# Kernel optimization log

Measured on AMD Instinct MI355X. Metric: run time of the kernel, lower is better.

Reference implementation:

```python
import jax, jax.numpy as jnp
import numpy as np
from jax import lax


def setup_inputs() -> dict:
    key = jax.random.key(0)
    ks = jax.random.split(key, 6)
    B, S, I, H = 64, 2048, 512, 512
    stdv = 1.0 / np.sqrt(H)
    return {
        "inputs": jax.random.normal(ks[0], (B, S, I), dtype=jnp.float32),
        "state": jax.random.normal(ks[1], (B, H), dtype=jnp.float32),
        "w_ih": jax.random.uniform(ks[2], (H, I), minval=-stdv, maxval=stdv, dtype=jnp.float32),
        "b_ih": jax.random.uniform(ks[3], (H, 1), minval=-stdv, maxval=stdv, dtype=jnp.float32),
        "w_hh": jax.random.uniform(ks[4], (H, H), minval=-stdv, maxval=stdv, dtype=jnp.float32),
        "b_hh": jax.random.uniform(ks[5], (H, 1), minval=-stdv, maxval=stdv, dtype=jnp.float32),
    }


def reference(inputs, state, w_ih, b_ih, w_hh, b_hh):
    """Tanh RNN: h_t = tanh(W_ih x_t + b_ih + W_hh h_{t-1} + b_hh).
    Returns (hidden_seq [S*B, H] (per-step states concatenated along dim 0,
    matching torch.cat(dim=0) in the original), h_last_T [H, B])."""
    B, S, I = inputs.shape
    H = w_hh.shape[0]
    # Hoist the input projection out of the recurrence: [B, S, H]
    x_proj = jnp.einsum('bsi,hi->bsh', inputs, w_ih) + (b_ih[:, 0] + b_hh[:, 0])

    def step(h, xp_t):  # h: [B, H], xp_t: [B, H]
        h_new = jnp.tanh(xp_t + h @ w_hh.T)
        return h_new, h_new

    h_last, hs = lax.scan(step, state, jnp.swapaxes(x_proj, 0, 1))  # hs: [S, B, H]
    hidden_seq = hs.reshape(S * B, H)
    return hidden_seq, h_last.T  # h_last.T matches the original's returned h_t of shape [H, B]
```

## Files before the change

kernel.cpp:

```cpp
#include <hip/hip_runtime.h>


typedef _Float16 half8 __attribute__((ext_vector_type(8)));
typedef _Float16 half4 __attribute__((ext_vector_type(4)));
typedef float f32x4 __attribute__((ext_vector_type(4)));
typedef unsigned long long u64;

#define S_SZ 2048
#define OUT1_OFF 67108864ull

#define XP_OFF    0ull
#define WHH_OFF   134217728ull
#define WIH_OFF   134742016ull
#define BIAS_OFF  135266304ull

#define WCHUNK    8208
#define NCHUNK    16
#define HSTRIDE   1072
#define HBUF_SZ   8576
#define WLDS_SZ   131328
#define SMEM_SZ   148480

__device__ __forceinline__ float fast_tanh(float x) {
    float a = exp2f(x * 2.8853900817779268f);
    return (a - 1.0f) * __builtin_amdgcn_rcpf(a + 1.0f);
}

__global__ void prep_kernel(const float* __restrict__ wih, const float* __restrict__ whh,
                            const float* __restrict__ bih, const float* __restrict__ bhh,
                            _Float16* __restrict__ wih16, _Float16* __restrict__ whh16,
                            float* __restrict__ bias)
{
    const int i = blockIdx.x * 256 + threadIdx.x;
    wih16[i] = (_Float16)wih[i];
    whh16[i] = (_Float16)whh[i];
    if (i < 512) bias[i] = bih[i] + bhh[i];
}

__global__ __launch_bounds__(512, 1) void xproj_kernel(
    const float* __restrict__ inputs, const _Float16* __restrict__ wih16,
    const float* __restrict__ bias, _Float16* __restrict__ xp16)
{
    __shared__ _Float16 Alds[64 * 512];
    const int s = blockIdx.x;

    for (int idx = threadIdx.x; idx < 64 * 128; idx += 512) {
        const int row = idx >> 7, chunk = idx & 127;
        const float4 v = *reinterpret_cast<const float4*>(
            inputs + ((size_t)row * S_SZ + s) * 512 + chunk * 4);
        half4 hv;
        hv[0] = (_Float16)v.x; hv[1] = (_Float16)v.y;
        hv[2] = (_Float16)v.z; hv[3] = (_Float16)v.w;
        const int bc = (chunk * 8) ^ ((row & 7) << 4);
        *reinterpret_cast<half4*>(reinterpret_cast<char*>(Alds) + row * 1024 + bc) = hv;
    }
    __syncthreads();

    const int lane = threadIdx.x & 63, w = threadIdx.x >> 6;
    const int l15 = lane & 15, lg = lane >> 4;

    f32x4 acc[4][4];
    #pragma unroll
    for (int m = 0; m < 4; ++m)
        #pragma unroll
        for (int n = 0; n < 4; ++n)
            acc[m][n] = 0.0f;

    for (int kk = 0; kk < 16; ++kk) {
        half8 af[4], bf[4];
        #pragma unroll
        for (int m = 0; m < 4; ++m) {
            const int row = m * 16 + l15;
            const int bc = (kk * 64 + lg * 16) ^ ((row & 7) << 4);
            af[m] = *reinterpret_cast<const half8*>(
                reinterpret_cast<const char*>(Alds) + row * 1024 + bc);
        }
        #pragma unroll
        for (int n = 0; n < 4; ++n) {
            const int col = w * 64 + n * 16 + l15;
            bf[n] = *reinterpret_cast<const half8*>(wih16 + (size_t)col * 512 + kk * 32 + lg * 8);
        }
        #pragma unroll
        for (int m = 0; m < 4; ++m)
            #pragma unroll
            for (int n = 0; n < 4; ++n)
                acc[m][n] = __builtin_amdgcn_mfma_f32_16x16x32_f16(bf[n], af[m], acc[m][n], 0, 0, 0);
    }

    #pragma unroll
    for (int m = 0; m < 4; ++m) {
        const int brow = m * 16 + l15;
        #pragma unroll
        for (int n = 0; n < 4; ++n) {
            const int j0 = w * 64 + n * 16 + lg * 4;
            const float4 bv = *reinterpret_cast<const float4*>(bias + j0);
            half4 hv;
            hv[0] = (_Float16)(acc[m][n][0] + bv.x);
            hv[1] = (_Float16)(acc[m][n][1] + bv.y);
            hv[2] = (_Float16)(acc[m][n][2] + bv.z);
            hv[3] = (_Float16)(acc[m][n][3] + bv.w);
            *reinterpret_cast<half4*>(xp16 + ((size_t)s * 64 + brow) * 512 + j0) = hv;
        }
    }
}

__global__ __launch_bounds__(256, 1) void rnn_step_kernel(
    const _Float16* __restrict__ whh16, const _Float16* __restrict__ xp16,
    const float* __restrict__ state, float* __restrict__ out)
{
    extern __shared__ __align__(16) char smem[];
    char* wlds   = smem;
    char* hbbase = smem + WLDS_SZ;

    const int r = blockIdx.x;
    const int tid = threadIdx.x;
    const int lane = tid & 63, w = tid >> 6;
    const int l15 = lane & 15, lg = lane >> 4;
    const int row8 = l15 & 7;
    const bool primary = (l15 < 8);

    for (int idx = tid; idx < NCHUNK * 512; idx += 256) {
        const int c = idx >> 9, j = idx & 511;
        const int kk = 12 + (c >> 2), lgc = c & 3;
        *reinterpret_cast<half8*>(wlds + c * WCHUNK + j * 16) =
            *reinterpret_cast<const half8*>(whh16 + (size_t)j * 512 + kk * 32 + lgc * 8);
    }
    for (int idx = tid; idx < 1024; idx += 256) {
        const int row = idx >> 7, jc = idx & 127;
        const float4 v = *reinterpret_cast<const float4*>(
            state + (size_t)(r * 8 + row) * 512 + jc * 4);
        half4 hv;
        hv[0] = (_Float16)v.x; hv[1] = (_Float16)v.y;
        hv[2] = (_Float16)v.z; hv[3] = (_Float16)v.w;
        *reinterpret_cast<half4*>(hbbase + row * HSTRIDE + jc * 8) = hv;
    }

    half8 wreg[96];
    {
        const _Float16* wp = whh16 + (size_t)(w * 128 + l15) * 512 + lg * 8;
        #pragma unroll
        for (int jt = 0; jt < 8; ++jt)
            #pragma unroll
            for (int kk = 0; kk < 12; ++kk)
                wreg[jt * 12 + kk] = *reinterpret_cast<const half8*>(wp + jt * 16 * 512 + kk * 32);
    }

    u64 xq[8];
    {
        const _Float16* xpb = xp16 + (size_t)(r * 8 + row8) * 512 + w * 128 + lg * 4;
        #pragma unroll
        for (int jt = 0; jt < 8; ++jt)
            xq[jt] = *reinterpret_cast<const u64*>(xpb + jt * 16);
    }

    __syncthreads();

    #pragma unroll 1
    for (int t = 0; t < S_SZ; ++t) {
        const char* hcur = hbbase + (t & 1) * HBUF_SZ;
        char* hnxt = hbbase + ((t + 1) & 1) * HBUF_SZ;

        f32x4 acc[8];
        #pragma unroll
        for (int jt = 0; jt < 8; ++jt) acc[jt] = 0.0f;

        #pragma unroll
        for (int kk = 0; kk < 12; ++kk) {
            const half8 bf = *reinterpret_cast<const half8*>(
                hcur + row8 * HSTRIDE + kk * 64 + lg * 16);
            #pragma unroll
            for (int jt = 0; jt < 8; ++jt)
                acc[jt] = __builtin_amdgcn_mfma_f32_16x16x32_f16(wreg[jt * 12 + kk], bf, acc[jt], 0, 0, 0);
        }
        #pragma unroll
        for (int kk = 12; kk < 16; ++kk) {
            const half8 bf = *reinterpret_cast<const half8*>(
                hcur + row8 * HSTRIDE + kk * 64 + lg * 16);
            const char* wc = wlds + ((kk - 12) * 4 + lg) * WCHUNK + (w * 128 + l15) * 16;
            #pragma unroll
            for (int jt = 0; jt < 8; ++jt) {
                const half8 a = *reinterpret_cast<const half8*>(wc + jt * 256);
                acc[jt] = __builtin_amdgcn_mfma_f32_16x16x32_f16(a, bf, acc[jt], 0, 0, 0);
            }
        }

        const int orow_idx = r * 8 + l15;
        float* orow = out + ((size_t)t * 64 + orow_idx) * 512 + w * 128 + lg * 4;
        #pragma unroll
        for (int jt = 0; jt < 8; ++jt) {
            union { _Float16 h[4]; u64 u; } xv, hp;
            xv.u = xq[jt];
            f32x4 f;
            #pragma unroll
            for (int q = 0; q < 4; ++q) {
                f[q] = fast_tanh(acc[jt][q] + (float)xv.h[q]);
                hp.h[q] = (_Float16)f[q];
            }
            if (primary) {
                *reinterpret_cast<u64*>(hnxt + l15 * HSTRIDE + (w * 128 + jt * 16 + lg * 4) * 2) = hp.u;
                *reinterpret_cast<f32x4*>(orow + jt * 16) = f;
                if (t == S_SZ - 1) {
                    const int j0 = w * 128 + jt * 16 + lg * 4;
                    #pragma unroll
                    for (int q = 0; q < 4; ++q)
                        out[OUT1_OFF + (size_t)(j0 + q) * 64 + orow_idx] = f[q];
                }
            }
        }

        if (t + 1 < S_SZ) {
            const _Float16* xpb = xp16 + ((size_t)(t + 1) * 64 + r * 8 + row8) * 512 + w * 128 + lg * 4;
            #pragma unroll
            for (int jt = 0; jt < 8; ++jt)
                xq[jt] = *reinterpret_cast<const u64*>(xpb + jt * 16);
        }

        __syncthreads();
    }
}

extern "C" void kernel_launch(void* const* d_in, const int* in_sizes, int n_in,
                              void* d_out, int out_size, void* d_ws, size_t ws_size,
                              hipStream_t stream)
{
    const float* inputs = (const float*)d_in[0];
    const float* state  = (const float*)d_in[1];
    const float* w_ih   = (const float*)d_in[2];
    const float* b_ih   = (const float*)d_in[3];
    const float* w_hh   = (const float*)d_in[4];
    const float* b_hh   = (const float*)d_in[5];
    float* out = (float*)d_out;
    char* ws = (char*)d_ws;

    _Float16* xp16  = (_Float16*)(ws + XP_OFF);
    _Float16* whh16 = (_Float16*)(ws + WHH_OFF);
    _Float16* wih16 = (_Float16*)(ws + WIH_OFF);
    float*    bias  = (float*)(ws + BIAS_OFF);

    hipFuncSetAttribute((const void*)rnn_step_kernel,
                        hipFuncAttributeMaxDynamicSharedMemorySize, SMEM_SZ);

    prep_kernel<<<1024, 256, 0, stream>>>(w_ih, w_hh, b_ih, b_hh, wih16, whh16, bias);
    xproj_kernel<<<S_SZ, 512, 0, stream>>>(inputs, wih16, bias, xp16);
    rnn_step_kernel<<<8, 256, SMEM_SZ, stream>>>(whh16, xp16, state, out);
}
```

Before: 7.686 ms.

## Pin recurrent weights in AGPRs and reorder hidden-state LDS layout for MFMA fragments

The register-resident W_hh slice is split into 64 half8 fragments forced into AGPRs via inline-asm constraints and 32 kept in VGPRs, instead of letting the compiler allocate all 96. The aim is to relieve VGPR pressure or spilling in the serial step loop. The hidden-state LDS buffer moves from a padded row-major layout to a fragment-ordered one, so each lane's B operand is a contiguous 16-byte read, and the W LDS chunks lose their padding. Risks include extra AGPR-to-VGPR moves before each MFMA and new LDS bank conflicts on the scattered 8-byte writes of the next state.

```diff
diff --git a/kernel.cpp b/kernel.cpp
--- a/kernel.cpp
+++ b/kernel.cpp
@@ -14,12 +14,9 @@
 #define WIH_OFF   134742016ull
 #define BIAS_OFF  135266304ull
 
-#define WCHUNK    8208
-#define NCHUNK    16
-#define HSTRIDE   1072
-#define HBUF_SZ   8576
-#define WLDS_SZ   131328
-#define SMEM_SZ   148480
+#define WLDS_SZ   131072
+#define HB_SZ     8192
+#define SMEM_SZ   147456
 
 __device__ __forceinline__ float fast_tanh(float x) {
     float a = exp2f(x * 2.8853900817779268f);
@@ -109,8 +106,8 @@
     const float* __restrict__ state, float* __restrict__ out)
 {
     extern __shared__ __align__(16) char smem[];
-    char* wlds   = smem;
-    char* hbbase = smem + WLDS_SZ;
+    char* wlds = smem;
+    char* hb   = smem + WLDS_SZ;
 
     const int r = blockIdx.x;
     const int tid = threadIdx.x;
@@ -119,31 +116,42 @@
     const int row8 = l15 & 7;
     const bool primary = (l15 < 8);
 
-    for (int idx = tid; idx < NCHUNK * 512; idx += 256) {
-        const int c = idx >> 9, j = idx & 511;
+    for (int idx = tid; idx < 16 * 512; idx += 256) {
+        const int c = idx >> 9, jj = idx & 511;
         const int kk = 12 + (c >> 2), lgc = c & 3;
-        *reinterpret_cast<half8*>(wlds + c * WCHUNK + j * 16) =
-            *reinterpret_cast<const half8*>(whh16 + (size_t)j * 512 + kk * 32 + lgc * 8);
-    }
-    for (int idx = tid; idx < 1024; idx += 256) {
-        const int row = idx >> 7, jc = idx & 127;
-        const float4 v = *reinterpret_cast<const float4*>(
-            state + (size_t)(r * 8 + row) * 512 + jc * 4);
-        half4 hv;
-        hv[0] = (_Float16)v.x; hv[1] = (_Float16)v.y;
-        hv[2] = (_Float16)v.z; hv[3] = (_Float16)v.w;
-        *reinterpret_cast<half4*>(hbbase + row * HSTRIDE + jc * 8) = hv;
-    }
-
-    half8 wreg[96];
+        *reinterpret_cast<half8*>(wlds + c * 8192 + jj * 16) =
+            *reinterpret_cast<const half8*>(whh16 + (size_t)jj * 512 + kk * 32 + lgc * 8);
+    }
+    for (int idx = tid; idx < 512; idx += 256) {
+        const int row = idx & 7, lgc = (idx >> 3) & 3, kk = idx >> 5;
+        const float* sp = state + (size_t)(r * 8 + row) * 512 + kk * 32 + lgc * 8;
+        const float4 v0 = *reinterpret_cast<const float4*>(sp);
+        const float4 v1 = *reinterpret_cast<const float4*>(sp + 4);
+        half8 hv;
+        hv[0] = (_Float16)v0.x; hv[1] = (_Float16)v0.y;
+        hv[2] = (_Float16)v0.z; hv[3] = (_Float16)v0.w;
+        hv[4] = (_Float16)v1.x; hv[5] = (_Float16)v1.y;
+        hv[6] = (_Float16)v1.z; hv[7] = (_Float16)v1.w;
+        *reinterpret_cast<half8*>(hb + ((kk * 4 + lgc) * 8 + row) * 16) = hv;
+    }
+
+    half8 wa[64], wv[32];
     {
         const _Float16* wp = whh16 + (size_t)(w * 128 + l15) * 512 + lg * 8;
         #pragma unroll
-        for (int jt = 0; jt < 8; ++jt)
-            #pragma unroll
-            for (int kk = 0; kk < 12; ++kk)
-                wreg[jt * 12 + kk] = *reinterpret_cast<const half8*>(wp + jt * 16 * 512 + kk * 32);
-    }
+        for (int jt = 0; jt < 8; ++jt) {
+            #pragma unroll
+            for (int kk = 0; kk < 8; ++kk)
+                wa[jt * 8 + kk] = *reinterpret_cast<const half8*>(wp + jt * 16 * 512 + kk * 32);
+            #pragma unroll
+            for (int kk = 8; kk < 12; ++kk)
+                wv[jt * 4 + kk - 8] = *reinterpret_cast<const half8*>(wp + jt * 16 * 512 + kk * 32);
+        }
+    }
+    #pragma unroll
+    for (int i = 0; i < 64; ++i) asm volatile("" : "+a"(wa[i]));
+    #pragma unroll
+    for (int i = 0; i < 32; ++i) asm volatile("" : "+v"(wv[i]));
 
     u64 xq[8];
     {
@@ -157,29 +165,40 @@
 
     #pragma unroll 1
     for (int t = 0; t < S_SZ; ++t) {
-        const char* hcur = hbbase + (t & 1) * HBUF_SZ;
-        char* hnxt = hbbase + ((t + 1) & 1) * HBUF_SZ;
+        const char* hc = hb + (t & 1) * HB_SZ;
+        char* hn = hb + ((t + 1) & 1) * HB_SZ;
 
         f32x4 acc[8];
         #pragma unroll
         for (int jt = 0; jt < 8; ++jt) acc[jt] = 0.0f;
 
         #pragma unroll
-        for (int kk = 0; kk < 12; ++kk) {
+        for (int kk = 0; kk < 8; ++kk) {
             const half8 bf = *reinterpret_cast<const half8*>(
-                hcur + row8 * HSTRIDE + kk * 64 + lg * 16);
+                hc + ((kk * 4 + lg) * 8 + row8) * 16);
             #pragma unroll
             for (int jt = 0; jt < 8; ++jt)
-                acc[jt] = __builtin_amdgcn_mfma_f32_16x16x32_f16(wreg[jt * 12 + kk], bf, acc[jt], 0, 0, 0);
+                acc[jt] = __builtin_amdgcn_mfma_f32_16x16x32_f16(
+                    wa[jt * 8 + kk], bf, acc[jt], 0, 0, 0);
+        }
+        #pragma unroll
+        for (int kk = 8; kk < 12; ++kk) {
+            const half8 bf = *reinterpret_cast<const half8*>(
+                hc + ((kk * 4 + lg) * 8 + row8) * 16);
+            #pragma unroll
+            for (int jt = 0; jt < 8; ++jt)
+                acc[jt] = __builtin_amdgcn_mfma_f32_16x16x32_f16(
+                    wv[jt * 4 + kk - 8], bf, acc[jt], 0, 0, 0);
         }
         #pragma unroll
         for (int kk = 12; kk < 16; ++kk) {
             const half8 bf = *reinterpret_cast<const half8*>(
-                hcur + row8 * HSTRIDE + kk * 64 + lg * 16);
-            const char* wc = wlds + ((kk - 12) * 4 + lg) * WCHUNK + (w * 128 + l15) * 16;
+                hc + ((kk * 4 + lg) * 8 + row8) * 16);
+            const char* wc = wlds + ((kk - 12) * 4 + lg) * 8192;
             #pragma unroll
             for (int jt = 0; jt < 8; ++jt) {
-                const half8 a = *reinterpret_cast<const half8*>(wc + jt * 256);
+                const half8 a = *reinterpret_cast<const half8*>(
+                    wc + (w * 128 + jt * 16 + l15) * 16);
                 acc[jt] = __builtin_amdgcn_mfma_f32_16x16x32_f16(a, bf, acc[jt], 0, 0, 0);
             }
         }
@@ -197,7 +216,8 @@
                 hp.h[q] = (_Float16)f[q];
             }
             if (primary) {
-                *reinterpret_cast<u64*>(hnxt + l15 * HSTRIDE + (w * 128 + jt * 16 + lg * 4) * 2) = hp.u;
+                const int e = ((w * 4 + (jt >> 1)) * 4 + 2 * (jt & 1) + (lg >> 1)) * 8 + l15;
+                *reinterpret_cast<u64*>(hn + e * 16 + (lg & 1) * 8) = hp.u;
                 *reinterpret_cast<f32x4*>(orow + jt * 16) = f;
                 if (t == S_SZ - 1) {
                     const int j0 = w * 128 + jt * 16 + lg * 4;
```

New measurement: 6.975 ms. 9.2% less time.
